# Performance work log

Hardware: AMD Instinct MI355X
Metric: run time of the kernel (lower is better)

Reference implementation:

```python
import jax, jax.numpy as jnp
import numpy as np

INT8_MAX = 127.0

def _quant_ste(x, axis):
    """Dynamic symmetric int8 fake-quant along `axis` (per-channel scales).
    Returns dequantized values; math matches int8 dot * scales (AQT-style)."""
    amax = jnp.max(jnp.abs(x), axis=axis, keepdims=True)
    scale = jnp.maximum(amax, 1e-6) / INT8_MAX
    q = jnp.clip(jnp.round(x / scale), -INT8_MAX, INT8_MAX)
    return q * scale

def setup_inputs() -> dict:
    key = jax.random.key(0)
    k1, k2 = jax.random.split(key)
    inputs = jax.random.normal(k1, (4, 2048, 4096), dtype=jnp.float32)
    kernel = jax.random.normal(k2, (4096, 4096), dtype=jnp.float32) * 0.02
    return {"inputs": inputs, "kernel": kernel}

def reference(inputs, kernel):
    # eqn: '...y,yz->...z' with quantized dot_general:
    # per-row (last-axis) dynamic int8 quant of activations,
    # per-output-column int8 quant of kernel, int8 matmul, dequant by scales.
    xq = _quant_ste(inputs, axis=-1)   # [B, S, D]
    kq = _quant_ste(kernel, axis=0)    # [D, F]
    return jnp.einsum('bsd,df->bsf', xq, kq)  # [B, S, F]
```

## Files before the change

### kernel.cpp

```cpp
#include <hip/hip_runtime.h>


#define M_DIM 8192
#define K_DIM 4096
#define N_DIM 4096

typedef int v4i __attribute__((ext_vector_type(4)));
typedef __attribute__((address_space(3))) void lds_void_t;
typedef const __attribute__((address_space(1))) void g_void_t;

__global__ void quant_act(const float* __restrict__ X,
                          signed char* __restrict__ Aq,
                          float* __restrict__ sx) {
  const int row = blockIdx.x;
  const int t = threadIdx.x;
  const float* xr = X + (size_t)row * K_DIM;
  float4 v[4];
  float am = 0.f;
#pragma unroll
  for (int c = 0; c < 4; ++c) {
    v[c] = ((const float4*)xr)[c * 256 + t];
    am = fmaxf(am, fmaxf(fmaxf(fabsf(v[c].x), fabsf(v[c].y)),
                         fmaxf(fabsf(v[c].z), fabsf(v[c].w))));
  }
#pragma unroll
  for (int off = 32; off > 0; off >>= 1)
    am = fmaxf(am, __shfl_down(am, off));
  __shared__ float red[4];
  __shared__ float s_inv;
  if ((t & 63) == 0) red[t >> 6] = am;
  __syncthreads();
  if (t == 0) {
    float m = fmaxf(fmaxf(red[0], red[1]), fmaxf(red[2], red[3]));
    float scale = fmaxf(m, 1e-6f) / 127.0f;
    sx[row] = scale;
    s_inv = 1.0f / scale;
  }
  __syncthreads();
  const float inv = s_inv;
  int* aq32 = (int*)(Aq + (size_t)row * K_DIM);
#pragma unroll
  for (int c = 0; c < 4; ++c) {
    int q0 = (int)fminf(fmaxf(rintf(v[c].x * inv), -127.f), 127.f);
    int q1 = (int)fminf(fmaxf(rintf(v[c].y * inv), -127.f), 127.f);
    int q2 = (int)fminf(fmaxf(rintf(v[c].z * inv), -127.f), 127.f);
    int q3 = (int)fminf(fmaxf(rintf(v[c].w * inv), -127.f), 127.f);
    aq32[c * 256 + t] = (q0 & 255) | ((q1 & 255) << 8) | ((q2 & 255) << 16) | (q3 << 24);
  }
}

__global__ void wk_amax_part(const float* __restrict__ Kmat, float* __restrict__ part) {
  const int f = blockIdx.x * 256 + threadIdx.x;
  const float* p = Kmat + (size_t)(blockIdx.y * 128) * N_DIM + f;
  float a0 = 0.f, a1 = 0.f, a2 = 0.f, a3 = 0.f;
#pragma unroll 4
  for (int i = 0; i < 32; ++i) {
    a0 = fmaxf(a0, fabsf(p[0 * N_DIM]));
    a1 = fmaxf(a1, fabsf(p[1 * N_DIM]));
    a2 = fmaxf(a2, fabsf(p[2 * N_DIM]));
    a3 = fmaxf(a3, fabsf(p[3 * N_DIM]));
    p += 4 * N_DIM;
  }
  part[(size_t)blockIdx.y * N_DIM + f] = fmaxf(fmaxf(a0, a1), fmaxf(a2, a3));
}

__global__ void wk_amax_comb(const float* __restrict__ part,
                             float* __restrict__ sk, float* __restrict__ skinv) {
  const int f = blockIdx.x * 256 + threadIdx.x;
  float am = 0.f;
#pragma unroll
  for (int s = 0; s < 32; ++s) am = fmaxf(am, part[(size_t)s * N_DIM + f]);
  float scale = fmaxf(am, 1e-6f) / 127.0f;
  sk[f] = scale;
  skinv[f] = 1.0f / scale;
}

__global__ void wk_quant(const float* __restrict__ Kmat,
                         const float* __restrict__ skinv,
                         signed char* __restrict__ BqT) {
  const int f0 = (blockIdx.x & 63) * 64;
  const int d0 = (blockIdx.x >> 6) * 64;
  const int t = threadIdx.x;
  const int fl = t & 63;
  const int dl0 = t >> 6;
  __shared__ signed char tile[64 * 68];
  const float inv = skinv[f0 + fl];
#pragma unroll
  for (int c = 0; c < 16; ++c) {
    const int dl = c * 4 + dl0;
    float vv = Kmat[(size_t)(d0 + dl) * N_DIM + f0 + fl];
    float q = fminf(fmaxf(rintf(vv * inv), -127.f), 127.f);
    tile[fl * 68 + dl] = (signed char)(int)q;
  }
  __syncthreads();
#pragma unroll
  for (int c = 0; c < 4; ++c) {
    const int idx = c * 256 + t;
    const int fr = idx >> 4;
    const int d4 = idx & 15;
    unsigned int w = *(const unsigned int*)&tile[fr * 68 + d4 * 4];
    *(unsigned int*)&BqT[(size_t)(f0 + fr) * K_DIM + d0 + d4 * 4] = w;
  }
}

__global__ __launch_bounds__(256, 2) void gemm_i8(
    const signed char* __restrict__ Aq, const signed char* __restrict__ BqT,
    const float* __restrict__ sx, const float* __restrict__ sk,
    float* __restrict__ C) {
  const int n0 = blockIdx.x * 128;
  const int m0 = blockIdx.y * 128;
  const int t = threadIdx.x;
  const int lane = t & 63;
  const int wave = t >> 6;
  const int wm = (wave >> 1) * 64;
  const int wn = (wave & 1) * 64;
  const int lrow = lane & 15;
  const int lq = lane >> 4;

  __shared__ __align__(16) signed char lA[128 * 64];
  __shared__ __align__(16) signed char lB[128 * 64];

  v4i acc[4][4];
#pragma unroll
  for (int i = 0; i < 4; ++i)
#pragma unroll
    for (int j = 0; j < 4; ++j) acc[i][j] = (v4i){0, 0, 0, 0};

  const signed char* Abase = Aq + (size_t)m0 * K_DIM;
  const signed char* Bbase = BqT + (size_t)n0 * K_DIM;

  int aoff[4], boff[4];
#pragma unroll
  for (int i = 0; i < 4; ++i) {
    aoff[i] = (wm + i * 16 + lrow) * 64 + lq * 16;
    boff[i] = (wn + i * 16 + lrow) * 64 + lq * 16;
  }

  for (int kb = 0; kb < K_DIM; kb += 64) {
#pragma unroll
    for (int c = 0; c < 2; ++c) {
      const int i = c * 256 + t;
      const int r = i >> 2;
      const int kc = (i & 3) * 16;
      __builtin_amdgcn_global_load_lds(
          (g_void_t*)(Abase + (size_t)r * K_DIM + kb + kc),
          (lds_void_t*)(lA + i * 16), 16, 0, 0);
      __builtin_amdgcn_global_load_lds(
          (g_void_t*)(Bbase + (size_t)r * K_DIM + kb + kc),
          (lds_void_t*)(lB + i * 16), 16, 0, 0);
    }
    __syncthreads();
    v4i af[4], bf[4];
#pragma unroll
    for (int i = 0; i < 4; ++i) af[i] = *(const v4i*)(lA + aoff[i]);
#pragma unroll
    for (int i = 0; i < 4; ++i) bf[i] = *(const v4i*)(lB + boff[i]);
#pragma unroll
    for (int mi = 0; mi < 4; ++mi)
#pragma unroll
      for (int ni = 0; ni < 4; ++ni)
        acc[mi][ni] =
            __builtin_amdgcn_mfma_i32_16x16x64_i8(af[mi], bf[ni], acc[mi][ni], 0, 0, 0);
    __syncthreads();
  }

#pragma unroll
  for (int mi = 0; mi < 4; ++mi) {
#pragma unroll
    for (int ni = 0; ni < 4; ++ni) {
      const int gn = n0 + wn + ni * 16 + lrow;
      const float skv = sk[gn];
#pragma unroll
      for (int r = 0; r < 4; ++r) {
        const int gm = m0 + wm + mi * 16 + lq * 4 + r;
        C[(size_t)gm * N_DIM + gn] = (float)acc[mi][ni][r] * sx[gm] * skv;
      }
    }
  }
}

extern "C" void kernel_launch(void* const* d_in, const int* in_sizes, int n_in,
                              void* d_out, int out_size, void* d_ws, size_t ws_size,
                              hipStream_t stream) {
  const float* X = (const float*)d_in[0];
  const float* W = (const float*)d_in[1];
  float* out = (float*)d_out;
  char* ws = (char*)d_ws;

  signed char* Aq = (signed char*)ws;
  signed char* BqT = (signed char*)(ws + 33554432);
  float* sx = (float*)(ws + 50331648);
  float* sk = (float*)(ws + 50364416);
  float* skinv = (float*)(ws + 50380800);
  float* part = (float*)(ws + 50397184);

  quant_act<<<M_DIM, 256, 0, stream>>>(X, Aq, sx);
  wk_amax_part<<<dim3(16, 32), 256, 0, stream>>>(W, part);
  wk_amax_comb<<<16, 256, 0, stream>>>(part, sk, skinv);
  wk_quant<<<4096, 256, 0, stream>>>(W, skinv, BqT);
  gemm_i8<<<dim3(N_DIM / 128, M_DIM / 128), 256, 0, stream>>>(Aq, BqT, sx, sk, out);
}
```

Before: 433.3 us.

## Pre-tile int8 operands into MFMA fragment order and double K-step per barrier

The quantization kernels now write A and B in a 16-row-by-16-byte tiled layout that matches the MFMA fragment order, so the GEMM's LDS fills are contiguous 16-byte chunks and fragment reads are lane-contiguous without bank conflicts. The GEMM main loop also processes 128 K per barrier pair instead of 64, using 32KB of LDS. This halves the synchronization count and aims to cut LDS conflicts and scattered global loads, at the cost of more LDS use per block, which may limit occupancy, and a shuffle step in quant_act.

Result: faster. 419.1 us (-3.3%).

```diff
diff --git a/kernel.cpp b/kernel.cpp
--- a/kernel.cpp
+++ b/kernel.cpp
@@ -10,7 +10,7 @@
 typedef const __attribute__((address_space(1))) void g_void_t;
 
 __global__ void quant_act(const float* __restrict__ X,
-                          signed char* __restrict__ Aq,
+                          signed char* __restrict__ At,
                           float* __restrict__ sx) {
   const int row = blockIdx.x;
   const int t = threadIdx.x;
@@ -28,6 +28,7 @@
     am = fmaxf(am, __shfl_down(am, off));
   __shared__ float red[4];
   __shared__ float s_inv;
+  __shared__ unsigned int shuf[1024];
   if ((t & 63) == 0) red[t >> 6] = am;
   __syncthreads();
   if (t == 0) {
@@ -38,15 +39,18 @@
   }
   __syncthreads();
   const float inv = s_inv;
-  int* aq32 = (int*)(Aq + (size_t)row * K_DIM);
 #pragma unroll
   for (int c = 0; c < 4; ++c) {
     int q0 = (int)fminf(fmaxf(rintf(v[c].x * inv), -127.f), 127.f);
     int q1 = (int)fminf(fmaxf(rintf(v[c].y * inv), -127.f), 127.f);
     int q2 = (int)fminf(fmaxf(rintf(v[c].z * inv), -127.f), 127.f);
     int q3 = (int)fminf(fmaxf(rintf(v[c].w * inv), -127.f), 127.f);
-    aq32[c * 256 + t] = (q0 & 255) | ((q1 & 255) << 8) | ((q2 & 255) << 16) | (q3 << 24);
-  }
+    shuf[c * 256 + t] = (q0 & 255) | ((q1 & 255) << 8) | ((q2 & 255) << 16) | (q3 << 24);
+  }
+  __syncthreads();
+  v4i w = *(const v4i*)&shuf[t * 4];
+  signed char* dst = At + (size_t)(row >> 4) * 65536 + t * 256 + (row & 15) * 16;
+  *(v4i*)dst = w;
 }
 
 __global__ void wk_amax_part(const float* __restrict__ Kmat, float* __restrict__ part) {
@@ -77,34 +81,32 @@
 
 __global__ void wk_quant(const float* __restrict__ Kmat,
                          const float* __restrict__ skinv,
-                         signed char* __restrict__ BqT) {
+                         signed char* __restrict__ Bt) {
   const int f0 = (blockIdx.x & 63) * 64;
   const int d0 = (blockIdx.x >> 6) * 64;
   const int t = threadIdx.x;
   const int fl = t & 63;
   const int dl0 = t >> 6;
-  __shared__ signed char tile[64 * 68];
+  __shared__ __align__(16) signed char tile[64 * 80];
   const float inv = skinv[f0 + fl];
 #pragma unroll
   for (int c = 0; c < 16; ++c) {
     const int dl = c * 4 + dl0;
     float vv = Kmat[(size_t)(d0 + dl) * N_DIM + f0 + fl];
     float q = fminf(fmaxf(rintf(vv * inv), -127.f), 127.f);
-    tile[fl * 68 + dl] = (signed char)(int)q;
-  }
-  __syncthreads();
-#pragma unroll
-  for (int c = 0; c < 4; ++c) {
-    const int idx = c * 256 + t;
-    const int fr = idx >> 4;
-    const int d4 = idx & 15;
-    unsigned int w = *(const unsigned int*)&tile[fr * 68 + d4 * 4];
-    *(unsigned int*)&BqT[(size_t)(f0 + fr) * K_DIM + d0 + d4 * 4] = w;
-  }
+    tile[fl * 80 + dl] = (signed char)(int)q;
+  }
+  __syncthreads();
+  const int frow = t >> 2;
+  const int ksl = t & 3;
+  v4i w = *(const v4i*)&tile[frow * 80 + ksl * 16];
+  const int f = f0 + frow;
+  signed char* dst = Bt + (size_t)(f >> 4) * 65536 + ((d0 >> 4) + ksl) * 256 + (f & 15) * 16;
+  *(v4i*)dst = w;
 }
 
 __global__ __launch_bounds__(256, 2) void gemm_i8(
-    const signed char* __restrict__ Aq, const signed char* __restrict__ BqT,
+    const signed char* __restrict__ At, const signed char* __restrict__ Bt,
     const float* __restrict__ sx, const float* __restrict__ sk,
     float* __restrict__ C) {
   const int n0 = blockIdx.x * 128;
@@ -117,8 +119,9 @@
   const int lrow = lane & 15;
   const int lq = lane >> 4;
 
-  __shared__ __align__(16) signed char lA[128 * 64];
-  __shared__ __align__(16) signed char lB[128 * 64];
+  __shared__ __align__(16) signed char lds[32768];
+  signed char* lA = lds;
+  signed char* lB = lds + 16384;
 
   v4i acc[4][4];
 #pragma unroll
@@ -126,41 +129,41 @@
 #pragma unroll
     for (int j = 0; j < 4; ++j) acc[i][j] = (v4i){0, 0, 0, 0};
 
-  const signed char* Abase = Aq + (size_t)m0 * K_DIM;
-  const signed char* Bbase = BqT + (size_t)n0 * K_DIM;
-
-  int aoff[4], boff[4];
-#pragma unroll
-  for (int i = 0; i < 4; ++i) {
-    aoff[i] = (wm + i * 16 + lrow) * 64 + lq * 16;
-    boff[i] = (wn + i * 16 + lrow) * 64 + lq * 16;
-  }
-
-  for (int kb = 0; kb < K_DIM; kb += 64) {
-#pragma unroll
-    for (int c = 0; c < 2; ++c) {
-      const int i = c * 256 + t;
-      const int r = i >> 2;
-      const int kc = (i & 3) * 16;
+  const signed char* Abase = At + (size_t)(m0 >> 4) * 65536;
+  const signed char* Bbase = Bt + (size_t)(n0 >> 4) * 65536;
+
+  const int la = ((wave >> 1) * 4) * 2048 + lane * 16;
+  const int lb = ((wave & 1) * 4) * 2048 + lane * 16;
+
+  for (int kb = 0; kb < K_DIM; kb += 128) {
+    const int kofs = kb * 16;
+#pragma unroll
+    for (int j = 0; j < 4; ++j) {
+      const int c = j * 256 + t;
+      const int mt_i = c >> 7;
+      const int inner = c & 127;
       __builtin_amdgcn_global_load_lds(
-          (g_void_t*)(Abase + (size_t)r * K_DIM + kb + kc),
-          (lds_void_t*)(lA + i * 16), 16, 0, 0);
+          (g_void_t*)(Abase + (size_t)mt_i * 65536 + kofs + inner * 16),
+          (lds_void_t*)(lA + c * 16), 16, 0, 0);
       __builtin_amdgcn_global_load_lds(
-          (g_void_t*)(Bbase + (size_t)r * K_DIM + kb + kc),
-          (lds_void_t*)(lB + i * 16), 16, 0, 0);
+          (g_void_t*)(Bbase + (size_t)mt_i * 65536 + kofs + inner * 16),
+          (lds_void_t*)(lB + c * 16), 16, 0, 0);
     }
     __syncthreads();
-    v4i af[4], bf[4];
-#pragma unroll
-    for (int i = 0; i < 4; ++i) af[i] = *(const v4i*)(lA + aoff[i]);
-#pragma unroll
-    for (int i = 0; i < 4; ++i) bf[i] = *(const v4i*)(lB + boff[i]);
-#pragma unroll
-    for (int mi = 0; mi < 4; ++mi)
-#pragma unroll
-      for (int ni = 0; ni < 4; ++ni)
-        acc[mi][ni] =
-            __builtin_amdgcn_mfma_i32_16x16x64_i8(af[mi], bf[ni], acc[mi][ni], 0, 0, 0);
+#pragma unroll
+    for (int s = 0; s < 2; ++s) {
+      v4i af[4], bf[4];
+#pragma unroll
+      for (int i = 0; i < 4; ++i) af[i] = *(const v4i*)(lA + la + i * 2048 + s * 1024);
+#pragma unroll
+      for (int i = 0; i < 4; ++i) bf[i] = *(const v4i*)(lB + lb + i * 2048 + s * 1024);
+#pragma unroll
+      for (int mi = 0; mi < 4; ++mi)
+#pragma unroll
+        for (int ni = 0; ni < 4; ++ni)
+          acc[mi][ni] =
+              __builtin_amdgcn_mfma_i32_16x16x64_i8(af[mi], bf[ni], acc[mi][ni], 0, 0, 0);
+    }
     __syncthreads();
   }
 
@@ -187,16 +190,16 @@
   float* out = (float*)d_out;
   char* ws = (char*)d_ws;
 
-  signed char* Aq = (signed char*)ws;
-  signed char* BqT = (signed char*)(ws + 33554432);
+  signed char* At = (signed char*)ws;
+  signed char* Bt = (signed char*)(ws + 33554432);
   float* sx = (float*)(ws + 50331648);
   float* sk = (float*)(ws + 50364416);
   float* skinv = (float*)(ws + 50380800);
   float* part = (float*)(ws + 50397184);
 
-  quant_act<<<M_DIM, 256, 0, stream>>>(X, Aq, sx);
+  quant_act<<<M_DIM, 256, 0, stream>>>(X, At, sx);
   wk_amax_part<<<dim3(16, 32), 256, 0, stream>>>(W, part);
   wk_amax_comb<<<16, 256, 0, stream>>>(part, sk, skinv);
-  wk_quant<<<4096, 256, 0, stream>>>(W, skinv, BqT);
-  gemm_i8<<<dim3(N_DIM / 128, M_DIM / 128), 256, 0, stream>>>(Aq, BqT, sx, sk, out);
-}
+  wk_quant<<<4096, 256, 0, stream>>>(W, skinv, Bt);
+  gemm_i8<<<dim3(N_DIM / 128, M_DIM / 128), 256, 0, stream>>>(At, Bt, sx, sk, out);
+}
```
